# Performance work log

Measured on AMD Instinct MI355X. Metric: run time of the kernel, lower is better.

Reference implementation:

```python
import jax, jax.numpy as jnp
import numpy as np

B, D, H, W = 16, 512, 32, 32   # batch, input_dim, spatial
CD, K = 256, 8192              # codebook dim, num codes
COMMIT = 1.0


def setup_inputs() -> dict:
    key = jax.random.key(0)
    k0, k1, k2, k3 = jax.random.split(key, 4)
    x = jax.random.normal(k0, (B, D, H, W), dtype=jnp.float32)
    # project_in: Linear(D -> CD); project_out: Linear(CD -> D)
    W_in = jax.random.normal(k1, (CD, D), dtype=jnp.float32) * (1.0 / np.sqrt(D))
    b_in = jnp.zeros((CD,), dtype=jnp.float32)
    W_out = jax.random.normal(k2, (D, CD), dtype=jnp.float32) * (1.0 / np.sqrt(CD))
    b_out = jnp.zeros((D,), dtype=jnp.float32)
    codebook = jax.random.normal(k3, (K, CD), dtype=jnp.float32) * 0.05
    return {"x": x, "W_in": W_in, "b_in": b_in, "W_out": W_out,
            "b_out": b_out, "codebook": codebook}


def reference(x, W_in, b_in, W_out, b_out, codebook):
    b, d, h, w = x.shape
    # b d h w -> b (h w) d
    xt = x.reshape(b, d, h * w).transpose(0, 2, 1)
    z = xt @ W_in.T + b_in                              # [b, n, CD]
    # squared euclidean distances to all codes: ||z||^2 - 2 z.e + ||e||^2
    d2 = ((z * z).sum(-1, keepdims=True)
          - 2.0 * jnp.einsum('bnc,kc->bnk', z, codebook)
          + (codebook * codebook).sum(-1))              # [b, n, K]
    indices = jnp.argmin(d2, axis=-1)                   # [b, n] int
    q = codebook[indices]                               # [b, n, CD]
    # training branch: commitment loss + straight-through estimator
    commitment_loss = COMMIT * jnp.mean((jax.lax.stop_gradient(q) - z) ** 2)
    q_ste = z + jax.lax.stop_gradient(q - z)
    out = q_ste @ W_out.T + b_out                       # [b, n, d]
    out = out.transpose(0, 2, 1).reshape(b, d, h, w)    # b (h w) d -> b d h w
    return out, indices, commitment_loss
```

## Files before the change

kernel.cpp:

```cpp
#include <hip/hip_runtime.h>
#include <cfloat>
#include <cstdint>

#define B_      16
#define DIN     512
#define HW      1024
#define CDIM    256
#define KCODES  8192
#define NTOK    (B_ * HW)
#define OUT_ELEMS (B_ * DIN * HW)
#define GAP_EPS 1e-3f
#define NSTRIP  8
#define NPART   (NSTRIP * 2)
#define CPS     (KCODES / NSTRIP)
#define MAXR    4096
#define RCHUNK  32
#define RBLOCKS 2048
#define LOSS_SCALE (1.0f / ((float)NTOK * (float)CDIM))

typedef __attribute__((ext_vector_type(8))) short bf16x8;
typedef __attribute__((ext_vector_type(4))) float f32x4;

static __device__ __forceinline__ short f2bf(float f) {
  unsigned u = __builtin_bit_cast(unsigned, f);
  u += 0x7FFFu + ((u >> 16) & 1u);
  return (short)(u >> 16);
}
static __device__ __forceinline__ float bf2f(short h) {
  unsigned u = ((unsigned)(unsigned short)h) << 16;
  return __builtin_bit_cast(float, u);
}

#define GLL16(gsrc, ldst)                                                      \
  __builtin_amdgcn_global_load_lds(                                            \
      (const __attribute__((address_space(1))) unsigned int*)(gsrc),           \
      (__attribute__((address_space(3))) unsigned int*)(ldst), 16, 0, 0)

#define PREP_CB_BLKS 2048
#define PREP_W_BLKS  128
#define PREP_X_BLKS  2048
__global__ __launch_bounds__(256) void k_prep(
    const float* __restrict__ cb, const float* __restrict__ Win,
    const float* __restrict__ Wout, const float* __restrict__ x,
    short* __restrict__ cb_hi, short* __restrict__ cb_lo, float* __restrict__ ee,
    short* __restrict__ wi_hi, short* __restrict__ wi_lo,
    short* __restrict__ wo_hi, short* __restrict__ wo_lo,
    short* __restrict__ xT_hi, short* __restrict__ xT_lo,
    float* __restrict__ loss, int* __restrict__ rcount) {
  __shared__ float T[64][65];
  const int blk = blockIdx.x;
  const int tid = threadIdx.x;
  if (blk == 0 && tid < 2) {
    if (tid == 0) *loss = 0.0f; else *rcount = 0;
  }
  if (blk < PREP_CB_BLKS) {
    const int wid = (blk * 256 + tid) >> 6;
    const int lane = tid & 63;
    const float4 v = *(const float4*)(cb + (size_t)wid * CDIM + lane * 4);
    float s = v.x * v.x + v.y * v.y + v.z * v.z + v.w * v.w;
    short4 h, l;
    h.x = f2bf(v.x); l.x = f2bf(v.x - bf2f(h.x));
    h.y = f2bf(v.y); l.y = f2bf(v.y - bf2f(h.y));
    h.z = f2bf(v.z); l.z = f2bf(v.z - bf2f(h.z));
    h.w = f2bf(v.w); l.w = f2bf(v.w - bf2f(h.w));
    *(short4*)(cb_hi + (size_t)wid * CDIM + lane * 4) = h;
    *(short4*)(cb_lo + (size_t)wid * CDIM + lane * 4) = l;
#pragma unroll
    for (int off = 32; off > 0; off >>= 1) s += __shfl_down(s, off, 64);
    if (lane == 0) ee[wid] = s;
  } else if (blk < PREP_CB_BLKS + PREP_W_BLKS) {
    const int i = ((blk - PREP_CB_BLKS) * 256 + tid) * 4;
    {
      const float4 v = *(const float4*)(Win + i);
      short4 h, l;
      h.x = f2bf(v.x); l.x = f2bf(v.x - bf2f(h.x));
      h.y = f2bf(v.y); l.y = f2bf(v.y - bf2f(h.y));
      h.z = f2bf(v.z); l.z = f2bf(v.z - bf2f(h.z));
      h.w = f2bf(v.w); l.w = f2bf(v.w - bf2f(h.w));
      *(short4*)(wi_hi + i) = h; *(short4*)(wi_lo + i) = l;
    }
    {
      const float4 v = *(const float4*)(Wout + i);
      short4 h, l;
      h.x = f2bf(v.x); l.x = f2bf(v.x - bf2f(h.x));
      h.y = f2bf(v.y); l.y = f2bf(v.y - bf2f(h.y));
      h.z = f2bf(v.z); l.z = f2bf(v.z - bf2f(h.z));
      h.w = f2bf(v.w); l.w = f2bf(v.w - bf2f(h.w));
      *(short4*)(wo_hi + i) = h; *(short4*)(wo_lo + i) = l;
    }
  } else {
    const int id = blk - PREP_CB_BLKS - PREP_W_BLKS;
    const int xb = id & 255, yb = id >> 8;
    const int b = xb >> 4;
    const int hw0 = (xb & 15) * 64;
    const int din0 = yb * 64;
    {
      const int r = tid >> 2;
      const int c = tid & 3;
      const float* src = x + ((size_t)b * DIN + din0 + r) * HW + hw0 + c * 16;
#pragma unroll
      for (int j = 0; j < 4; ++j) {
        const float4 v = *(const float4*)(src + j * 4);
        T[r][c * 16 + j * 4 + 0] = v.x;
        T[r][c * 16 + j * 4 + 1] = v.y;
        T[r][c * 16 + j * 4 + 2] = v.z;
        T[r][c * 16 + j * 4 + 3] = v.w;
      }
    }
    __syncthreads();
    {
      const int tt = tid & 63;
      const int c2 = tid >> 6;
      short h[16], l[16];
#pragma unroll
      for (int j = 0; j < 16; ++j) {
        const float f = T[c2 * 16 + j][tt];
        h[j] = f2bf(f); l[j] = f2bf(f - bf2f(h[j]));
      }
      const size_t base = ((size_t)b * HW + hw0 + tt) * DIN + din0 + c2 * 16;
      *(bf16x8*)(xT_hi + base)     = *(bf16x8*)&h[0];
      *(bf16x8*)(xT_hi + base + 8) = *(bf16x8*)&h[8];
      *(bf16x8*)(xT_lo + base)     = *(bf16x8*)&l[0];
      *(bf16x8*)(xT_lo + base + 8) = *(bf16x8*)&l[8];
    }
  }
}

__global__ __launch_bounds__(256, 2) void k_proj_in_mfma(
    const short* __restrict__ xT_hi, const short* __restrict__ xT_lo,
    const short* __restrict__ wi_hi, const short* __restrict__ wi_lo,
    const float* __restrict__ bin,
    short* __restrict__ z_hi, short* __restrict__ z_lo) {
  __shared__ short lds_s[4 * 128 * 32];
  char* ldsc = (char*)lds_s;
  const int tid = threadIdx.x;
  const int w = tid >> 6, lane = tid & 63;
  const int quad = lane >> 4, l16 = lane & 15;
  const int wm = w >> 1, wn = w & 1;
  const int tok0 = blockIdx.x * 128;
  const int cd0 = blockIdx.y * 128;

  const int uA = (w << 6) + lane, uB = uA + 256;
  const int tA = uA >> 2, pA = uA & 3, qA = pA ^ ((tA >> 1) & 3);
  const int tB = uB >> 2, pB = uB & 3, qB = pB ^ ((tB >> 1) & 3);
  const int offA = tA * DIN + qA * 8;
  const int offB = tB * DIN + qB * 8;
  const short* gAh0 = xT_hi + (size_t)tok0 * DIN + offA;
  const short* gAh1 = xT_hi + (size_t)tok0 * DIN + offB;
  const short* gAl0 = xT_lo + (size_t)tok0 * DIN + offA;
  const short* gAl1 = xT_lo + (size_t)tok0 * DIN + offB;
  const short* gBh0 = wi_hi + (size_t)cd0 * DIN + offA;
  const short* gBh1 = wi_hi + (size_t)cd0 * DIN + offB;
  const short* gBl0 = wi_lo + (size_t)cd0 * DIN + offA;
  const short* gBl1 = wi_lo + (size_t)cd0 * DIN + offB;

  int aoffs[4], boffs[4];
#pragma unroll
  for (int mi = 0; mi < 4; ++mi) {
    const int t = wm * 64 + mi * 16 + l16;
    aoffs[mi] = t * 64 + (quad ^ ((t >> 1) & 3)) * 16;
  }
#pragma unroll
  for (int ni = 0; ni < 4; ++ni) {
    const int t = wn * 64 + ni * 16 + l16;
    boffs[ni] = 16384 + t * 64 + (quad ^ ((t >> 1) & 3)) * 16;
  }

  f32x4 acc[4][4];
#pragma unroll
  for (int mi = 0; mi < 4; ++mi)
#pragma unroll
    for (int ni = 0; ni < 4; ++ni) acc[mi][ni] = (f32x4){0.f, 0.f, 0.f, 0.f};

  for (int kb = 0; kb < DIN; kb += 32) {
    __syncthreads();
    GLL16(gAh0 + kb, ldsc + ((0 * 4 + w) << 10));
    GLL16(gAh1 + kb, ldsc + ((1 * 4 + w) << 10));
    GLL16(gAl0 + kb, ldsc + ((2 * 4 + w) << 10));
    GLL16(gAl1 + kb, ldsc + ((3 * 4 + w) << 10));
    GLL16(gBh0 + kb, ldsc + ((4 * 4 + w) << 10));
    GLL16(gBh1 + kb, ldsc + ((5 * 4 + w) << 10));
    GLL16(gBl0 + kb, ldsc + ((6 * 4 + w) << 10));
    GLL16(gBl1 + kb, ldsc + ((7 * 4 + w) << 10));
    __syncthreads();
    bf16x8 ah[4], al[4], bh[4], bl[4];
#pragma unroll
    for (int mi = 0; mi < 4; ++mi) {
      ah[mi] = *(const bf16x8*)(ldsc + aoffs[mi]);
      al[mi] = *(const bf16x8*)(ldsc + 8192 + aoffs[mi]);
    }
#pragma unroll
    for (int ni = 0; ni < 4; ++ni) {
      bh[ni] = *(const bf16x8*)(ldsc + boffs[ni]);
      bl[ni] = *(const bf16x8*)(ldsc + 8192 + boffs[ni]);
    }
#pragma unroll
    for (int mi = 0; mi < 4; ++mi)
#pragma unroll
      for (int ni = 0; ni < 4; ++ni) {
        f32x4 c = acc[mi][ni];
        c = __builtin_amdgcn_mfma_f32_16x16x32_bf16(ah[mi], bh[ni], c, 0, 0, 0);
        c = __builtin_amdgcn_mfma_f32_16x16x32_bf16(ah[mi], bl[ni], c, 0, 0, 0);
        c = __builtin_amdgcn_mfma_f32_16x16x32_bf16(al[mi], bh[ni], c, 0, 0, 0);
        acc[mi][ni] = c;
      }
  }
  float bv[4];
#pragma unroll
  for (int ni = 0; ni < 4; ++ni) bv[ni] = bin[cd0 + wn * 64 + ni * 16 + l16];
#pragma unroll
  for (int mi = 0; mi < 4; ++mi)
#pragma unroll
    for (int r = 0; r < 4; ++r) {
      const int t = tok0 + wm * 64 + mi * 16 + quad * 4 + r;
#pragma unroll
      for (int ni = 0; ni < 4; ++ni) {
        const int cd = cd0 + wn * 64 + ni * 16 + l16;
        const float o = acc[mi][ni][r] + bv[ni];
        const short h = f2bf(o);
        z_hi[(size_t)t * CDIM + cd] = h;
        z_lo[(size_t)t * CDIM + cd] = f2bf(o - bf2f(h));
      }
    }
}

__global__ __launch_bounds__(256, 2) void k_argmin_mfma(
    const short* __restrict__ z_hi, const short* __restrict__ z_lo,
    const short* __restrict__ cb_hi, const short* __restrict__ cb_lo,
    const float* __restrict__ ee,
    float* __restrict__ pmv, int* __restrict__ pmi, float* __restrict__ psv) {
  __shared__ short lds_s[4 * 128 * 32];
  char* ldsc = (char*)lds_s;
  const int tid = threadIdx.x;
  const int w = tid >> 6, lane = tid & 63;
  const int quad = lane >> 4, l16 = lane & 15;
  const int wm = w >> 1, wn = w & 1;
  const int tok0 = blockIdx.x * 128;
  const int cbase = blockIdx.y * CPS;

  const int uA = (w << 6) + lane, uB = uA + 256;
  const int tA = uA >> 2, pA = uA & 3, qA = pA ^ ((tA >> 1) & 3);
  const int tB = uB >> 2, pB = uB & 3, qB = pB ^ ((tB >> 1) & 3);
  const int offA = tA * CDIM + qA * 8;
  const int offB = tB * CDIM + qB * 8;
  const short* gAh0 = z_hi + (size_t)tok0 * CDIM + offA;
  const short* gAh1 = z_hi + (size_t)tok0 * CDIM + offB;
  const short* gAl0 = z_lo + (size_t)tok0 * CDIM + offA;
  const short* gAl1 = z_lo + (size_t)tok0 * CDIM + offB;

  int aoffs[4], boffs[4];
#pragma unroll
  for (int mi = 0; mi < 4; ++mi) {
    const int t = wm * 64 + mi * 16 + l16;
    aoffs[mi] = t * 64 + (quad ^ ((t >> 1) & 3)) * 16;
  }
#pragma unroll
  for (int ni = 0; ni < 4; ++ni) {
    const int t = wn * 64 + ni * 16 + l16;
    boffs[ni] = 16384 + t * 64 + (quad ^ ((t >> 1) & 3)) * 16;
  }

  float mv[16], sv[16]; int bidx[16];
#pragma unroll
  for (int j = 0; j < 16; ++j) { mv[j] = FLT_MAX; sv[j] = FLT_MAX; bidx[j] = 0; }

  for (int ct = 0; ct < CPS / 128; ++ct) {
    const int ctile = cbase + ct * 128;
    const short* gBh0 = cb_hi + (size_t)ctile * CDIM + offA;
    const short* gBh1 = cb_hi + (size_t)ctile * CDIM + offB;
    const short* gBl0 = cb_lo + (size_t)ctile * CDIM + offA;
    const short* gBl1 = cb_lo + (size_t)ctile * CDIM + offB;
    f32x4 acc[4][4];
#pragma unroll
    for (int mi = 0; mi < 4; ++mi)
#pragma unroll
      for (int ni = 0; ni < 4; ++ni) acc[mi][ni] = (f32x4){0.f, 0.f, 0.f, 0.f};

    for (int kb = 0; kb < CDIM; kb += 32) {
      __syncthreads();
      GLL16(gAh0 + kb, ldsc + ((0 * 4 + w) << 10));
      GLL16(gAh1 + kb, ldsc + ((1 * 4 + w) << 10));
      GLL16(gAl0 + kb, ldsc + ((2 * 4 + w) << 10));
      GLL16(gAl1 + kb, ldsc + ((3 * 4 + w) << 10));
      GLL16(gBh0 + kb, ldsc + ((4 * 4 + w) << 10));
      GLL16(gBh1 + kb, ldsc + ((5 * 4 + w) << 10));
      GLL16(gBl0 + kb, ldsc + ((6 * 4 + w) << 10));
      GLL16(gBl1 + kb, ldsc + ((7 * 4 + w) << 10));
      __syncthreads();
      bf16x8 ah[4], al[4], bh[4], bl[4];
#pragma unroll
      for (int mi = 0; mi < 4; ++mi) {
        ah[mi] = *(const bf16x8*)(ldsc + aoffs[mi]);
        al[mi] = *(const bf16x8*)(ldsc + 8192 + aoffs[mi]);
      }
#pragma unroll
      for (int ni = 0; ni < 4; ++ni) {
        bh[ni] = *(const bf16x8*)(ldsc + boffs[ni]);
        bl[ni] = *(const bf16x8*)(ldsc + 8192 + boffs[ni]);
      }
#pragma unroll
      for (int mi = 0; mi < 4; ++mi)
#pragma unroll
        for (int ni = 0; ni < 4; ++ni) {
          f32x4 c = acc[mi][ni];
          c = __builtin_amdgcn_mfma_f32_16x16x32_bf16(ah[mi], bh[ni], c, 0, 0, 0);
          c = __builtin_amdgcn_mfma_f32_16x16x32_bf16(ah[mi], bl[ni], c, 0, 0, 0);
          c = __builtin_amdgcn_mfma_f32_16x16x32_bf16(al[mi], bh[ni], c, 0, 0, 0);
          acc[mi][ni] = c;
        }
    }
    float eev[4];
#pragma unroll
    for (int ni = 0; ni < 4; ++ni) eev[ni] = ee[ctile + wn * 64 + ni * 16 + l16];
    const int cb2 = ctile + wn * 64 + l16;
#pragma unroll
    for (int mi = 0; mi < 4; ++mi)
#pragma unroll
      for (int r = 0; r < 4; ++r) {
        const int j = mi * 4 + r;
#pragma unroll
        for (int ni = 0; ni < 4; ++ni) {
          const float s = fmaf(-2.0f, acc[mi][ni][r], eev[ni]);
          sv[j] = fminf(sv[j], fmaxf(mv[j], s));
          if (s < mv[j]) { mv[j] = s; bidx[j] = cb2 + ni * 16; }
        }
      }
  }
#pragma unroll
  for (int off = 1; off < 16; off <<= 1) {
#pragma unroll
    for (int j = 0; j < 16; ++j) {
      const float ov = __shfl_xor(mv[j], off, 64);
      const int   oi = __shfl_xor(bidx[j], off, 64);
      const float os = __shfl_xor(sv[j], off, 64);
      const float snew = fminf(fminf(sv[j], os), fmaxf(mv[j], ov));
      if (ov < mv[j] || (ov == mv[j] && oi < bidx[j])) { mv[j] = ov; bidx[j] = oi; }
      sv[j] = snew;
    }
  }
  if (l16 == 0) {
    const int strip = blockIdx.y * 2 + wn;
#pragma unroll
    for (int j = 0; j < 16; ++j) {
      const int mi = j >> 2, r = j & 3;
      const int t = tok0 + wm * 64 + mi * 16 + quad * 4 + r;
      const size_t o = (size_t)strip * NTOK + t;
      pmv[o] = mv[j]; pmi[o] = bidx[j]; psv[o] = sv[j];
    }
  }
}

__global__ __launch_bounds__(256) void k_merge_loss(
    const float* __restrict__ pmv, const int* __restrict__ pmi,
    const float* __restrict__ psv,
    const short* __restrict__ z_hi, const short* __restrict__ z_lo,
    const float* __restrict__ cb,
    int* __restrict__ idxi, float* __restrict__ idx_f,
    int* __restrict__ rlist, int* __restrict__ rcount,
    float* __restrict__ loss) {
  __shared__ float lpart[4];
  const int tid = threadIdx.x;
  const int wv = tid >> 6, lane = tid & 63;
  const int t = blockIdx.x * 4 + wv;
  float mv = FLT_MAX, sv = FLT_MAX; int mi = 0x7fffffff;
  if (lane < NPART) {
    mv = pmv[(size_t)lane * NTOK + t];
    mi = pmi[(size_t)lane * NTOK + t];
    sv = psv[(size_t)lane * NTOK + t];
  }
#pragma unroll
  for (int off = 1; off < 16; off <<= 1) {
    const float ov = __shfl_xor(mv, off, 64);
    const int   oi = __shfl_xor(mi, off, 64);
    const float os = __shfl_xor(sv, off, 64);
    const float snew = fminf(fminf(sv, os), fmaxf(mv, ov));
    if (ov < mv || (ov == mv && oi < mi)) { mv = ov; mi = oi; }
    sv = snew;
  }
  const int mif = __shfl(mi, 0, 64);
  const short4 h4 = *(const short4*)(z_hi + (size_t)t * CDIM + lane * 4);
  const short4 l4 = *(const short4*)(z_lo + (size_t)t * CDIM + lane * 4);
  const float4 qv = *(const float4*)(cb + (size_t)mif * CDIM + lane * 4);
  const float dx = qv.x - (bf2f(h4.x) + bf2f(l4.x));
  const float dy = qv.y - (bf2f(h4.y) + bf2f(l4.y));
  const float dz = qv.z - (bf2f(h4.z) + bf2f(l4.z));
  const float dw = qv.w - (bf2f(h4.w) + bf2f(l4.w));
  float s = dx * dx + dy * dy + dz * dz + dw * dw;
#pragma unroll
  for (int off = 32; off > 0; off >>= 1) s += __shfl_down(s, off, 64);
  if (lane == 0) {
    idxi[t] = mif;
    idx_f[t] = (float)mif;
    lpart[wv] = s;
    if (sv - mv < GAP_EPS) {
      const int pos = atomicAdd(rcount, 1);
      if (pos < MAXR) rlist[pos] = t;
    }
  }
  __syncthreads();
  if (tid == 0) {
    atomicAdd(loss, (lpart[0] + lpart[1] + lpart[2] + lpart[3]) * LOSS_SCALE);
  }
}

__global__ __launch_bounds__(256) void k_rescue_chunk(
    const short* __restrict__ z_hi, const short* __restrict__ z_lo,
    const float* __restrict__ cb,
    const int* __restrict__ rlist, const int* __restrict__ rcount,
    double* __restrict__ slotv, int* __restrict__ sloti) {
  const int cnt0 = *rcount;
  const int cnt = cnt0 < MAXR ? cnt0 : MAXR;
  const int li0 = blockIdx.x >> 5;
  const int chunk = blockIdx.x & (RCHUNK - 1);
  if (li0 >= cnt) return;
  __shared__ float zrow[CDIM];
  __shared__ double rv[256];
  __shared__ int ri[256];
  const int tid = threadIdx.x;
  for (int li = li0; li < cnt; li += RBLOCKS / RCHUNK) {
    const int t = rlist[li];
    zrow[tid] = bf2f(z_hi[(size_t)t * CDIM + tid]) + bf2f(z_lo[(size_t)t * CDIM + tid]);
    __syncthreads();
    const int k = chunk * 256 + tid;
    const float* e = cb + (size_t)k * CDIM;
    double s0 = 0.0, s1 = 0.0, s2 = 0.0, s3 = 0.0;
    for (int c = 0; c < CDIM; c += 4) {
      const double d0 = (double)zrow[c]     - (double)e[c];
      const double d1 = (double)zrow[c + 1] - (double)e[c + 1];
      const double d2 = (double)zrow[c + 2] - (double)e[c + 2];
      const double d3 = (double)zrow[c + 3] - (double)e[c + 3];
      s0 += d0 * d0; s1 += d1 * d1; s2 += d2 * d2; s3 += d3 * d3;
    }
    rv[tid] = (s0 + s1) + (s2 + s3);
    ri[tid] = k;
    __syncthreads();
    for (int off = 128; off > 0; off >>= 1) {
      if (tid < off) {
        if (rv[tid + off] < rv[tid] ||
            (rv[tid + off] == rv[tid] && ri[tid + off] < ri[tid])) {
          rv[tid] = rv[tid + off]; ri[tid] = ri[tid + off];
        }
      }
      __syncthreads();
    }
    if (tid == 0) {
      slotv[(size_t)li * RCHUNK + chunk] = rv[0];
      sloti[(size_t)li * RCHUNK + chunk] = ri[0];
    }
    __syncthreads();
  }
}

__global__ __launch_bounds__(256) void k_rescue_fin(
    const double* __restrict__ slotv, const int* __restrict__ sloti,
    const int* __restrict__ rlist, const int* __restrict__ rcount,
    const short* __restrict__ z_hi, const short* __restrict__ z_lo,
    const float* __restrict__ cb,
    int* __restrict__ idxi, float* __restrict__ idx_f, float* __restrict__ loss) {
  const int cnt0 = *rcount;
  const int cnt = cnt0 < MAXR ? cnt0 : MAXR;
  const int tid = threadIdx.x;
  const int wv = tid >> 6, lane = tid & 63;
  for (int li = wv; li < cnt; li += 4) {
    double bv = 1e300; int bx = 0x7fffffff;
    if (lane < RCHUNK) {
      bv = slotv[(size_t)li * RCHUNK + lane];
      bx = sloti[(size_t)li * RCHUNK + lane];
    }
#pragma unroll
    for (int off = 1; off < 32; off <<= 1) {
      const double ov = __shfl_xor(bv, off, 64);
      const int   oi = __shfl_xor(bx, off, 64);
      if (ov < bv || (ov == bv && oi < bx)) { bv = ov; bx = oi; }
    }
    const int newi = __shfl(bx, 0, 64);
    const int t = rlist[li];
    const int oldi = idxi[t];
    if (newi != oldi) {
      const short4 h4 = *(const short4*)(z_hi + (size_t)t * CDIM + lane * 4);
      const short4 l4 = *(const short4*)(z_lo + (size_t)t * CDIM + lane * 4);
      const float4 qn = *(const float4*)(cb + (size_t)newi * CDIM + lane * 4);
      const float4 qo = *(const float4*)(cb + (size_t)oldi * CDIM + lane * 4);
      const float zx = bf2f(h4.x) + bf2f(l4.x);
      const float zy = bf2f(h4.y) + bf2f(l4.y);
      const float zz = bf2f(h4.z) + bf2f(l4.z);
      const float zw = bf2f(h4.w) + bf2f(l4.w);
      float d = (qn.x - zx) * (qn.x - zx) - (qo.x - zx) * (qo.x - zx)
              + (qn.y - zy) * (qn.y - zy) - (qo.y - zy) * (qo.y - zy)
              + (qn.z - zz) * (qn.z - zz) - (qo.z - zz) * (qo.z - zz)
              + (qn.w - zw) * (qn.w - zw) - (qo.w - zw) * (qo.w - zw);
#pragma unroll
      for (int off = 32; off > 0; off >>= 1) d += __shfl_down(d, off, 64);
      if (lane == 0) {
        idxi[t] = newi;
        idx_f[t] = (float)newi;
        atomicAdd(loss, d * LOSS_SCALE);
      }
    }
  }
}

__global__ __launch_bounds__(256, 2) void k_proj_out_mfma(
    const short* __restrict__ wo_hi, const short* __restrict__ wo_lo,
    const short* __restrict__ cb_hi, const short* __restrict__ cb_lo,
    const int* __restrict__ idxi, const float* __restrict__ bout,
    float* __restrict__ out) {
  __shared__ short lds_s[4 * 128 * 32];
  char* ldsc = (char*)lds_s;
  const int tid = threadIdx.x;
  const int w = tid >> 6, lane = tid & 63;
  const int quad = lane >> 4, l16 = lane & 15;
  const int wm = w >> 1, wn = w & 1;
  const int tok0 = blockIdx.x * 128;
  const int din0 = blockIdx.y * 128;

  const int uA = (w << 6) + lane, uB = uA + 256;
  const int tA = uA >> 2, pA = uA & 3, qA = pA ^ ((tA >> 1) & 3);
  const int tB = uB >> 2, pB = uB & 3, qB = pB ^ ((tB >> 1) & 3);
  const short* gAh0 = wo_hi + (size_t)(din0 + tA) * CDIM + qA * 8;
  const short* gAh1 = wo_hi + (size_t)(din0 + tB) * CDIM + qB * 8;
  const short* gAl0 = wo_lo + (size_t)(din0 + tA) * CDIM + qA * 8;
  const short* gAl1 = wo_lo + (size_t)(din0 + tB) * CDIM + qB * 8;
  const int iA = idxi[tok0 + tA];
  const int iB = idxi[tok0 + tB];
  const short* gBh0 = cb_hi + (size_t)iA * CDIM + qA * 8;
  const short* gBh1 = cb_hi + (size_t)iB * CDIM + qB * 8;
  const short* gBl0 = cb_lo + (size_t)iA * CDIM + qA * 8;
  const short* gBl1 = cb_lo + (size_t)iB * CDIM + qB * 8;

  int aoffs[4], boffs[4];
#pragma unroll
  for (int mi = 0; mi < 4; ++mi) {
    const int t = wm * 64 + mi * 16 + l16;
    aoffs[mi] = t * 64 + (quad ^ ((t >> 1) & 3)) * 16;
  }
#pragma unroll
  for (int ni = 0; ni < 4; ++ni) {
    const int t = wn * 64 + ni * 16 + l16;
    boffs[ni] = 16384 + t * 64 + (quad ^ ((t >> 1) & 3)) * 16;
  }

  f32x4 acc[4][4];
#pragma unroll
  for (int mi = 0; mi < 4; ++mi)
#pragma unroll
    for (int ni = 0; ni < 4; ++ni) acc[mi][ni] = (f32x4){0.f, 0.f, 0.f, 0.f};

  for (int kb = 0; kb < CDIM; kb += 32) {
    __syncthreads();
    GLL16(gAh0 + kb, ldsc + ((0 * 4 + w) << 10));
    GLL16(gAh1 + kb, ldsc + ((1 * 4 + w) << 10));
    GLL16(gAl0 + kb, ldsc + ((2 * 4 + w) << 10));
    GLL16(gAl1 + kb, ldsc + ((3 * 4 + w) << 10));
    GLL16(gBh0 + kb, ldsc + ((4 * 4 + w) << 10));
    GLL16(gBh1 + kb, ldsc + ((5 * 4 + w) << 10));
    GLL16(gBl0 + kb, ldsc + ((6 * 4 + w) << 10));
    GLL16(gBl1 + kb, ldsc + ((7 * 4 + w) << 10));
    __syncthreads();
    bf16x8 ah[4], al[4], bh[4], bl[4];
#pragma unroll
    for (int mi = 0; mi < 4; ++mi) {
      ah[mi] = *(const bf16x8*)(ldsc + aoffs[mi]);
      al[mi] = *(const bf16x8*)(ldsc + 8192 + aoffs[mi]);
    }
#pragma unroll
    for (int ni = 0; ni < 4; ++ni) {
      bh[ni] = *(const bf16x8*)(ldsc + boffs[ni]);
      bl[ni] = *(const bf16x8*)(ldsc + 8192 + boffs[ni]);
    }
#pragma unroll
    for (int mi = 0; mi < 4; ++mi)
#pragma unroll
      for (int ni = 0; ni < 4; ++ni) {
        f32x4 c = acc[mi][ni];
        c = __builtin_amdgcn_mfma_f32_16x16x32_bf16(ah[mi], bh[ni], c, 0, 0, 0);
        c = __builtin_amdgcn_mfma_f32_16x16x32_bf16(ah[mi], bl[ni], c, 0, 0, 0);
        c = __builtin_amdgcn_mfma_f32_16x16x32_bf16(al[mi], bh[ni], c, 0, 0, 0);
        acc[mi][ni] = c;
      }
  }
  const int b = tok0 >> 10;
  const int hwb = tok0 & (HW - 1);
  float* ob = out + (size_t)b * DIN * HW;
#pragma unroll
  for (int mi = 0; mi < 4; ++mi)
#pragma unroll
    for (int r = 0; r < 4; ++r) {
      const int din = din0 + wm * 64 + mi * 16 + quad * 4 + r;
      const float bb = bout[din];
#pragma unroll
      for (int ni = 0; ni < 4; ++ni) {
        const int hw = hwb + wn * 64 + ni * 16 + l16;
        ob[(size_t)din * HW + hw] = acc[mi][ni][r] + bb;
      }
    }
}

extern "C" void kernel_launch(void* const* d_in, const int* in_sizes, int n_in,
                              void* d_out, int out_size, void* d_ws, size_t ws_size,
                              hipStream_t stream) {
  const float* x    = (const float*)d_in[0];
  const float* Win  = (const float*)d_in[1];
  const float* bin  = (const float*)d_in[2];
  const float* Wout = (const float*)d_in[3];
  const float* bout = (const float*)d_in[4];
  const float* cb   = (const float*)d_in[5];

  float* out   = (float*)d_out;
  float* idx_f = out + OUT_ELEMS;
  float* loss  = out + OUT_ELEMS + NTOK;

  char* w = (char*)d_ws;
  size_t off = 0;
  short* z_hi  = (short*)(w + off); off += (size_t)NTOK * CDIM * 2;
  short* z_lo  = (short*)(w + off); off += (size_t)NTOK * CDIM * 2;
  short* cb_hi = (short*)(w + off); off += (size_t)KCODES * CDIM * 2;
  short* cb_lo = (short*)(w + off); off += (size_t)KCODES * CDIM * 2;
  short* xT_hi = (short*)(w + off); off += (size_t)NTOK * DIN * 2;
  short* xT_lo = (short*)(w + off); off += (size_t)NTOK * DIN * 2;
  short* wi_hi = (short*)(w + off); off += (size_t)CDIM * DIN * 2;
  short* wi_lo = (short*)(w + off); off += (size_t)CDIM * DIN * 2;
  short* wo_hi = (short*)(w + off); off += (size_t)DIN * CDIM * 2;
  short* wo_lo = (short*)(w + off); off += (size_t)DIN * CDIM * 2;
  float* ee    = (float*)(w + off); off += (size_t)KCODES * 4;
  int*   idxi  = (int*)(w + off);   off += (size_t)NTOK * 4;
  float* pmv   = (float*)(w + off); off += (size_t)NPART * NTOK * 4;
  int*   pmi   = (int*)(w + off);   off += (size_t)NPART * NTOK * 4;
  float* psv   = (float*)(w + off); off += (size_t)NPART * NTOK * 4;
  int*   rlist = (int*)(w + off);   off += (size_t)MAXR * 4;
  int*   rcount= (int*)(w + off);   off += 256;
  double* slotv= (double*)(w + off);off += (size_t)MAXR * RCHUNK * 8;
  int*   sloti = (int*)(w + off);   off += (size_t)MAXR * RCHUNK * 4;

  k_prep        <<<dim3(PREP_CB_BLKS + PREP_W_BLKS + PREP_X_BLKS),
                   dim3(256), 0, stream>>>(cb, Win, Wout, x, cb_hi, cb_lo, ee,
                                           wi_hi, wi_lo, wo_hi, wo_lo,
                                           xT_hi, xT_lo, loss, rcount);
  k_proj_in_mfma<<<dim3(NTOK / 128, CDIM / 128), dim3(256), 0, stream>>>(
      xT_hi, xT_lo, wi_hi, wi_lo, bin, z_hi, z_lo);
  k_argmin_mfma <<<dim3(NTOK / 128, NSTRIP), dim3(256), 0, stream>>>(
      z_hi, z_lo, cb_hi, cb_lo, ee, pmv, pmi, psv);
  k_merge_loss  <<<dim3(NTOK / 4), dim3(256), 0, stream>>>(
      pmv, pmi, psv, z_hi, z_lo, cb, idxi, idx_f, rlist, rcount, loss);
  k_rescue_chunk<<<dim3(RBLOCKS), dim3(256), 0, stream>>>(
      z_hi, z_lo, cb, rlist, rcount, slotv, sloti);
  k_rescue_fin  <<<dim3(1), dim3(256), 0, stream>>>(
      slotv, sloti, rlist, rcount, z_hi, z_lo, cb, idxi, idx_f, loss);
  k_proj_out_mfma<<<dim3(NTOK / 128, DIN / 128), dim3(256), 0, stream>>>(
      wo_hi, wo_lo, cb_hi, cb_lo, idxi, bout, out);
}
```

Measured before the change: 467.0 us.

## Switch split-precision GEMMs from bf16 to scaled fp16 and drop low-part terms

```diff
diff --git a/kernel.cpp b/kernel.cpp
--- a/kernel.cpp
+++ b/kernel.cpp
@@ -9,31 +9,33 @@
 #define KCODES  8192
 #define NTOK    (B_ * HW)
 #define OUT_ELEMS (B_ * DIN * HW)
-#define GAP_EPS 1e-3f
+#define GAP_EPS 5e-3f
 #define NSTRIP  8
 #define NPART   (NSTRIP * 2)
 #define CPS     (KCODES / NSTRIP)
 #define MAXR    4096
 #define RCHUNK  32
-#define RBLOCKS 2048
+#define RBLOCKS 8192
 #define LOSS_SCALE (1.0f / ((float)NTOK * (float)CDIM))
-
-typedef __attribute__((ext_vector_type(8))) short bf16x8;
+#define WSCALE      16.0f
+#define INV_WS      0.0625f
+#define INV_WS2     0.00390625f
+#define NEG2_INV_WS (-0.125f)
+
+typedef __attribute__((ext_vector_type(8))) _Float16 f16x8;
 typedef __attribute__((ext_vector_type(4))) float f32x4;
 
-static __device__ __forceinline__ short f2bf(float f) {
-  unsigned u = __builtin_bit_cast(unsigned, f);
-  u += 0x7FFFu + ((u >> 16) & 1u);
-  return (short)(u >> 16);
-}
-static __device__ __forceinline__ float bf2f(short h) {
-  unsigned u = ((unsigned)(unsigned short)h) << 16;
-  return __builtin_bit_cast(float, u);
+static __device__ __forceinline__ short f2h(float f) {
+  _Float16 h = (_Float16)f;
+  return __builtin_bit_cast(short, h);
+}
+static __device__ __forceinline__ float h2f(short h) {
+  return (float)__builtin_bit_cast(_Float16, h);
 }
 
 #define GLL16(gsrc, ldst)                                                      \
-  __builtin_amdgcn_global_load_lds(                                            \
-      (const __attribute__((address_space(1))) unsigned int*)(gsrc),           \
+  __builtin_amdgcn_global_load_lds(                                           \
+      (const __attribute__((address_space(1))) unsigned int*)(gsrc),          \
       (__attribute__((address_space(3))) unsigned int*)(ldst), 16, 0, 0)
 
 #define PREP_CB_BLKS 2048
@@ -58,11 +60,13 @@
     const int lane = tid & 63;
     const float4 v = *(const float4*)(cb + (size_t)wid * CDIM + lane * 4);
     float s = v.x * v.x + v.y * v.y + v.z * v.z + v.w * v.w;
+    const float sx = v.x * WSCALE, sy = v.y * WSCALE,
+                sz = v.z * WSCALE, sw = v.w * WSCALE;
     short4 h, l;
-    h.x = f2bf(v.x); l.x = f2bf(v.x - bf2f(h.x));
-    h.y = f2bf(v.y); l.y = f2bf(v.y - bf2f(h.y));
-    h.z = f2bf(v.z); l.z = f2bf(v.z - bf2f(h.z));
-    h.w = f2bf(v.w); l.w = f2bf(v.w - bf2f(h.w));
+    h.x = f2h(sx); l.x = f2h(sx - h2f(h.x));
+    h.y = f2h(sy); l.y = f2h(sy - h2f(h.y));
+    h.z = f2h(sz); l.z = f2h(sz - h2f(h.z));
+    h.w = f2h(sw); l.w = f2h(sw - h2f(h.w));
     *(short4*)(cb_hi + (size_t)wid * CDIM + lane * 4) = h;
     *(short4*)(cb_lo + (size_t)wid * CDIM + lane * 4) = l;
 #pragma unroll
@@ -72,20 +76,24 @@
     const int i = ((blk - PREP_CB_BLKS) * 256 + tid) * 4;
     {
       const float4 v = *(const float4*)(Win + i);
+      const float sx = v.x * WSCALE, sy = v.y * WSCALE,
+                  sz = v.z * WSCALE, sw = v.w * WSCALE;
       short4 h, l;
-      h.x = f2bf(v.x); l.x = f2bf(v.x - bf2f(h.x));
-      h.y = f2bf(v.y); l.y = f2bf(v.y - bf2f(h.y));
-      h.z = f2bf(v.z); l.z = f2bf(v.z - bf2f(h.z));
-      h.w = f2bf(v.w); l.w = f2bf(v.w - bf2f(h.w));
+      h.x = f2h(sx); l.x = f2h(sx - h2f(h.x));
+      h.y = f2h(sy); l.y = f2h(sy - h2f(h.y));
+      h.z = f2h(sz); l.z = f2h(sz - h2f(h.z));
+      h.w = f2h(sw); l.w = f2h(sw - h2f(h.w));
       *(short4*)(wi_hi + i) = h; *(short4*)(wi_lo + i) = l;
     }
     {
       const float4 v = *(const float4*)(Wout + i);
+      const float sx = v.x * WSCALE, sy = v.y * WSCALE,
+                  sz = v.z * WSCALE, sw = v.w * WSCALE;
       short4 h, l;
-      h.x = f2bf(v.x); l.x = f2bf(v.x - bf2f(h.x));
-      h.y = f2bf(v.y); l.y = f2bf(v.y - bf2f(h.y));
-      h.z = f2bf(v.z); l.z = f2bf(v.z - bf2f(h.z));
-      h.w = f2bf(v.w); l.w = f2bf(v.w - bf2f(h.w));
+      h.x = f2h(sx); l.x = f2h(sx - h2f(h.x));
+      h.y = f2h(sy); l.y = f2h(sy - h2f(h.y));
+      h.z = f2h(sz); l.z = f2h(sz - h2f(h.z));
+      h.w = f2h(sw); l.w = f2h(sw - h2f(h.w));
       *(short4*)(wo_hi + i) = h; *(short4*)(wo_lo + i) = l;
     }
   } else {
@@ -115,13 +123,13 @@
 #pragma unroll
       for (int j = 0; j < 16; ++j) {
         const float f = T[c2 * 16 + j][tt];
-        h[j] = f2bf(f); l[j] = f2bf(f - bf2f(h[j]));
+        h[j] = f2h(f); l[j] = f2h(f - h2f(h[j]));
       }
       const size_t base = ((size_t)b * HW + hw0 + tt) * DIN + din0 + c2 * 16;
-      *(bf16x8*)(xT_hi + base)     = *(bf16x8*)&h[0];
-      *(bf16x8*)(xT_hi + base + 8) = *(bf16x8*)&h[8];
-      *(bf16x8*)(xT_lo + base)     = *(bf16x8*)&l[0];
-      *(bf16x8*)(xT_lo + base + 8) = *(bf16x8*)&l[8];
+      *(f16x8*)(xT_hi + base)     = *(f16x8*)&h[0];
+      *(f16x8*)(xT_hi + base + 8) = *(f16x8*)&h[8];
+      *(f16x8*)(xT_lo + base)     = *(f16x8*)&l[0];
+      *(f16x8*)(xT_lo + base + 8) = *(f16x8*)&l[8];
     }
   }
 }
@@ -183,25 +191,25 @@
     GLL16(gBl0 + kb, ldsc + ((6 * 4 + w) << 10));
     GLL16(gBl1 + kb, ldsc + ((7 * 4 + w) << 10));
     __syncthreads();
-    bf16x8 ah[4], al[4], bh[4], bl[4];
+    f16x8 ah[4], al[4], bh[4], bl[4];
 #pragma unroll
     for (int mi = 0; mi < 4; ++mi) {
-      ah[mi] = *(const bf16x8*)(ldsc + aoffs[mi]);
-      al[mi] = *(const bf16x8*)(ldsc + 8192 + aoffs[mi]);
+      ah[mi] = *(const f16x8*)(ldsc + aoffs[mi]);
+      al[mi] = *(const f16x8*)(ldsc + 8192 + aoffs[mi]);
     }
 #pragma unroll
     for (int ni = 0; ni < 4; ++ni) {
-      bh[ni] = *(const bf16x8*)(ldsc + boffs[ni]);
-      bl[ni] = *(const bf16x8*)(ldsc + 8192 + boffs[ni]);
+      bh[ni] = *(const f16x8*)(ldsc + boffs[ni]);
+      bl[ni] = *(const f16x8*)(ldsc + 8192 + boffs[ni]);
     }
 #pragma unroll
     for (int mi = 0; mi < 4; ++mi)
 #pragma unroll
       for (int ni = 0; ni < 4; ++ni) {
         f32x4 c = acc[mi][ni];
-        c = __builtin_amdgcn_mfma_f32_16x16x32_bf16(ah[mi], bh[ni], c, 0, 0, 0);
-        c = __builtin_amdgcn_mfma_f32_16x16x32_bf16(ah[mi], bl[ni], c, 0, 0, 0);
-        c = __builtin_amdgcn_mfma_f32_16x16x32_bf16(al[mi], bh[ni], c, 0, 0, 0);
+        c = __builtin_amdgcn_mfma_f32_16x16x32_f16(ah[mi], bh[ni], c, 0, 0, 0);
+        c = __builtin_amdgcn_mfma_f32_16x16x32_f16(ah[mi], bl[ni], c, 0, 0, 0);
+        c = __builtin_amdgcn_mfma_f32_16x16x32_f16(al[mi], bh[ni], c, 0, 0, 0);
         acc[mi][ni] = c;
       }
   }
@@ -216,20 +224,20 @@
 #pragma unroll
       for (int ni = 0; ni < 4; ++ni) {
         const int cd = cd0 + wn * 64 + ni * 16 + l16;
-        const float o = acc[mi][ni][r] + bv[ni];
-        const short h = f2bf(o);
+        const float o = acc[mi][ni][r] * INV_WS + bv[ni];
+        const short h = f2h(o);
         z_hi[(size_t)t * CDIM + cd] = h;
-        z_lo[(size_t)t * CDIM + cd] = f2bf(o - bf2f(h));
+        z_lo[(size_t)t * CDIM + cd] = f2h(o - h2f(h));
       }
     }
 }
 
 __global__ __launch_bounds__(256, 2) void k_argmin_mfma(
-    const short* __restrict__ z_hi, const short* __restrict__ z_lo,
+    const short* __restrict__ z_hi,
     const short* __restrict__ cb_hi, const short* __restrict__ cb_lo,
     const float* __restrict__ ee,
     float* __restrict__ pmv, int* __restrict__ pmi, float* __restrict__ psv) {
-  __shared__ short lds_s[4 * 128 * 32];
+  __shared__ short lds_s[3 * 128 * 32];
   char* ldsc = (char*)lds_s;
   const int tid = threadIdx.x;
   const int w = tid >> 6, lane = tid & 63;
@@ -245,8 +253,6 @@
   const int offB = tB * CDIM + qB * 8;
   const short* gAh0 = z_hi + (size_t)tok0 * CDIM + offA;
   const short* gAh1 = z_hi + (size_t)tok0 * CDIM + offB;
-  const short* gAl0 = z_lo + (size_t)tok0 * CDIM + offA;
-  const short* gAl1 = z_lo + (size_t)tok0 * CDIM + offB;
 
   int aoffs[4], boffs[4];
 #pragma unroll
@@ -257,7 +263,7 @@
 #pragma unroll
   for (int ni = 0; ni < 4; ++ni) {
     const int t = wn * 64 + ni * 16 + l16;
-    boffs[ni] = 16384 + t * 64 + (quad ^ ((t >> 1) & 3)) * 16;
+    boffs[ni] = 8192 + t * 64 + (quad ^ ((t >> 1) & 3)) * 16;
   }
 
   float mv[16], sv[16]; int bidx[16];
@@ -280,32 +286,27 @@
       __syncthreads();
       GLL16(gAh0 + kb, ldsc + ((0 * 4 + w) << 10));
       GLL16(gAh1 + kb, ldsc + ((1 * 4 + w) << 10));
-      GLL16(gAl0 + kb, ldsc + ((2 * 4 + w) << 10));
-      GLL16(gAl1 + kb, ldsc + ((3 * 4 + w) << 10));
-      GLL16(gBh0 + kb, ldsc + ((4 * 4 + w) << 10));
-      GLL16(gBh1 + kb, ldsc + ((5 * 4 + w) << 10));
-      GLL16(gBl0 + kb, ldsc + ((6 * 4 + w) << 10));
-      GLL16(gBl1 + kb, ldsc + ((7 * 4 + w) << 10));
+      GLL16(gBh0 + kb, ldsc + ((2 * 4 + w) << 10));
+      GLL16(gBh1 + kb, ldsc + ((3 * 4 + w) << 10));
+      GLL16(gBl0 + kb, ldsc + ((4 * 4 + w) << 10));
+      GLL16(gBl1 + kb, ldsc + ((5 * 4 + w) << 10));
       __syncthreads();
-      bf16x8 ah[4], al[4], bh[4], bl[4];
-#pragma unroll
-      for (int mi = 0; mi < 4; ++mi) {
-        ah[mi] = *(const bf16x8*)(ldsc + aoffs[mi]);
-        al[mi] = *(const bf16x8*)(ldsc + 8192 + aoffs[mi]);
-      }
+      f16x8 ah[4], bh[4], bl[4];
+#pragma unroll
+      for (int mi = 0; mi < 4; ++mi)
+        ah[mi] = *(const f16x8*)(ldsc + aoffs[mi]);
 #pragma unroll
       for (int ni = 0; ni < 4; ++ni) {
-        bh[ni] = *(const bf16x8*)(ldsc + boffs[ni]);
-        bl[ni] = *(const bf16x8*)(ldsc + 8192 + boffs[ni]);
+        bh[ni] = *(const f16x8*)(ldsc + boffs[ni]);
+        bl[ni] = *(const f16x8*)(ldsc + 8192 + boffs[ni]);
       }
 #pragma unroll
       for (int mi = 0; mi < 4; ++mi)
 #pragma unroll
         for (int ni = 0; ni < 4; ++ni) {
           f32x4 c = acc[mi][ni];
-          c = __builtin_amdgcn_mfma_f32_16x16x32_bf16(ah[mi], bh[ni], c, 0, 0, 0);
-          c = __builtin_amdgcn_mfma_f32_16x16x32_bf16(ah[mi], bl[ni], c, 0, 0, 0);
-          c = __builtin_amdgcn_mfma_f32_16x16x32_bf16(al[mi], bh[ni], c, 0, 0, 0);
+          c = __builtin_amdgcn_mfma_f32_16x16x32_f16(ah[mi], bh[ni], c, 0, 0, 0);
+          c = __builtin_amdgcn_mfma_f32_16x16x32_f16(ah[mi], bl[ni], c, 0, 0, 0);
           acc[mi][ni] = c;
         }
     }
@@ -320,7 +321,7 @@
         const int j = mi * 4 + r;
 #pragma unroll
         for (int ni = 0; ni < 4; ++ni) {
-          const float s = fmaf(-2.0f, acc[mi][ni][r], eev[ni]);
+          const float s = fmaf(NEG2_INV_WS, acc[mi][ni][r], eev[ni]);
           sv[j] = fminf(sv[j], fmaxf(mv[j], s));
           if (s < mv[j]) { mv[j] = s; bidx[j] = cb2 + ni * 16; }
         }
@@ -381,10 +382,10 @@
   const short4 h4 = *(const short4*)(z_hi + (size_t)t * CDIM + lane * 4);
   const short4 l4 = *(const short4*)(z_lo + (size_t)t * CDIM + lane * 4);
   const float4 qv = *(const float4*)(cb + (size_t)mif * CDIM + lane * 4);
-  const float dx = qv.x - (bf2f(h4.x) + bf2f(l4.x));
-  const float dy = qv.y - (bf2f(h4.y) + bf2f(l4.y));
-  const float dz = qv.z - (bf2f(h4.z) + bf2f(l4.z));
-  const float dw = qv.w - (bf2f(h4.w) + bf2f(l4.w));
+  const float dx = qv.x - (h2f(h4.x) + h2f(l4.x));
+  const float dy = qv.y - (h2f(h4.y) + h2f(l4.y));
+  const float dz = qv.z - (h2f(h4.z) + h2f(l4.z));
+  const float dw = qv.w - (h2f(h4.w) + h2f(l4.w));
   float s = dx * dx + dy * dy + dz * dz + dw * dw;
 #pragma unroll
   for (int off = 32; off > 0; off >>= 1) s += __shfl_down(s, off, 64);
@@ -419,16 +420,17 @@
   const int tid = threadIdx.x;
   for (int li = li0; li < cnt; li += RBLOCKS / RCHUNK) {
     const int t = rlist[li];
-    zrow[tid] = bf2f(z_hi[(size_t)t * CDIM + tid]) + bf2f(z_lo[(size_t)t * CDIM + tid]);
+    zrow[tid] = h2f(z_hi[(size_t)t * CDIM + tid]) + h2f(z_lo[(size_t)t * CDIM + tid]);
     __syncthreads();
     const int k = chunk * 256 + tid;
     const float* e = cb + (size_t)k * CDIM;
     double s0 = 0.0, s1 = 0.0, s2 = 0.0, s3 = 0.0;
     for (int c = 0; c < CDIM; c += 4) {
-      const double d0 = (double)zrow[c]     - (double)e[c];
-      const double d1 = (double)zrow[c + 1] - (double)e[c + 1];
-      const double d2 = (double)zrow[c + 2] - (double)e[c + 2];
-      const double d3 = (double)zrow[c + 3] - (double)e[c + 3];
+      const float4 ev = *(const float4*)(e + c);
+      const double d0 = (double)zrow[c]     - (double)ev.x;
+      const double d1 = (double)zrow[c + 1] - (double)ev.y;
+      const double d2 = (double)zrow[c + 2] - (double)ev.z;
+      const double d3 = (double)zrow[c + 3] - (double)ev.w;
       s0 += d0 * d0; s1 += d1 * d1; s2 += d2 * d2; s3 += d3 * d3;
     }
     rv[tid] = (s0 + s1) + (s2 + s3);
@@ -481,10 +483,10 @@
       const short4 l4 = *(const short4*)(z_lo + (size_t)t * CDIM + lane * 4);
       const float4 qn = *(const float4*)(cb + (size_t)newi * CDIM + lane * 4);
       const float4 qo = *(const float4*)(cb + (size_t)oldi * CDIM + lane * 4);
-      const float zx = bf2f(h4.x) + bf2f(l4.x);
-      const float zy = bf2f(h4.y) + bf2f(l4.y);
-      const float zz = bf2f(h4.z) + bf2f(l4.z);
-      const float zw = bf2f(h4.w) + bf2f(l4.w);
+      const float zx = h2f(h4.x) + h2f(l4.x);
+      const float zy = h2f(h4.y) + h2f(l4.y);
+      const float zz = h2f(h4.z) + h2f(l4.z);
+      const float zw = h2f(h4.w) + h2f(l4.w);
       float d = (qn.x - zx) * (qn.x - zx) - (qo.x - zx) * (qo.x - zx)
               + (qn.y - zy) * (qn.y - zy) - (qo.y - zy) * (qo.y - zy)
               + (qn.z - zz) * (qn.z - zz) - (qo.z - zz) * (qo.z - zz)
@@ -501,11 +503,11 @@
 }
 
 __global__ __launch_bounds__(256, 2) void k_proj_out_mfma(
-    const short* __restrict__ wo_hi, const short* __restrict__ wo_lo,
+    const short* __restrict__ wo_hi,
     const short* __restrict__ cb_hi, const short* __restrict__ cb_lo,
     const int* __restrict__ idxi, const float* __restrict__ bout,
     float* __restrict__ out) {
-  __shared__ short lds_s[4 * 128 * 32];
+  __shared__ short lds_s[3 * 128 * 32];
   char* ldsc = (char*)lds_s;
   const int tid = threadIdx.x;
   const int w = tid >> 6, lane = tid & 63;
@@ -519,8 +521,6 @@
   const int tB = uB >> 2, pB = uB & 3, qB = pB ^ ((tB >> 1) & 3);
   const short* gAh0 = wo_hi + (size_t)(din0 + tA) * CDIM + qA * 8;
   const short* gAh1 = wo_hi + (size_t)(din0 + tB) * CDIM + qB * 8;
-  const short* gAl0 = wo_lo + (size_t)(din0 + tA) * CDIM + qA * 8;
-  const short* gAl1 = wo_lo + (size_t)(din0 + tB) * CDIM + qB * 8;
   const int iA = idxi[tok0 + tA];
   const int iB = idxi[tok0 + tB];
   const short* gBh0 = cb_hi + (size_t)iA * CDIM + qA * 8;
@@ -537,7 +537,7 @@
 #pragma unroll
   for (int ni = 0; ni < 4; ++ni) {
     const int t = wn * 64 + ni * 16 + l16;
-    boffs[ni] = 16384 + t * 64 + (quad ^ ((t >> 1) & 3)) * 16;
+    boffs[ni] = 8192 + t * 64 + (quad ^ ((t >> 1) & 3)) * 16;
   }
 
   f32x4 acc[4][4];
@@ -550,32 +550,27 @@
     __syncthreads();
     GLL16(gAh0 + kb, ldsc + ((0 * 4 + w) << 10));
     GLL16(gAh1 + kb, ldsc + ((1 * 4 + w) << 10));
-    GLL16(gAl0 + kb, ldsc + ((2 * 4 + w) << 10));
-    GLL16(gAl1 + kb, ldsc + ((3 * 4 + w) << 10));
-    GLL16(gBh0 + kb, ldsc + ((4 * 4 + w) << 10));
-    GLL16(gBh1 + kb, ldsc + ((5 * 4 + w) << 10));
-    GLL16(gBl0 + kb, ldsc + ((6 * 4 + w) << 10));
-    GLL16(gBl1 + kb, ldsc + ((7 * 4 + w) << 10));
-    __syncthreads();
-    bf16x8 ah[4], al[4], bh[4], bl[4];
-#pragma unroll
-    for (int mi = 0; mi < 4; ++mi) {
-      ah[mi] = *(const bf16x8*)(ldsc + aoffs[mi]);
-      al[mi] = *(const bf16x8*)(ldsc + 8192 + aoffs[mi]);
-    }
+    GLL16(gBh0 + kb, ldsc + ((2 * 4 + w) << 10));
+    GLL16(gBh1 + kb, ldsc + ((3 * 4 + w) << 10));
+    GLL16(gBl0 + kb, ldsc + ((4 * 4 + w) << 10));
+    GLL16(gBl1 + kb, ldsc + ((5 * 4 + w) << 10));
+    __syncthreads();
+    f16x8 ah[4], bh[4], bl[4];
+#pragma unroll
+    for (int mi = 0; mi < 4; ++mi)
+      ah[mi] = *(const f16x8*)(ldsc + aoffs[mi]);
 #pragma unroll
     for (int ni = 0; ni < 4; ++ni) {
-      bh[ni] = *(const bf16x8*)(ldsc + boffs[ni]);
-      bl[ni] = *(const bf16x8*)(ldsc + 8192 + boffs[ni]);
+      bh[ni] = *(const f16x8*)(ldsc + boffs[ni]);
+      bl[ni] = *(const f16x8*)(ldsc + 8192 + boffs[ni]);
     }
 #pragma unroll
     for (int mi = 0; mi < 4; ++mi)
 #pragma unroll
       for (int ni = 0; ni < 4; ++ni) {
         f32x4 c = acc[mi][ni];
-        c = __builtin_amdgcn_mfma_f32_16x16x32_bf16(ah[mi], bh[ni], c, 0, 0, 0);
-        c = __builtin_amdgcn_mfma_f32_16x16x32_bf16(ah[mi], bl[ni], c, 0, 0, 0);
-        c = __builtin_amdgcn_mfma_f32_16x16x32_bf16(al[mi], bh[ni], c, 0, 0, 0);
+        c = __builtin_amdgcn_mfma_f32_16x16x32_f16(ah[mi], bh[ni], c, 0, 0, 0);
+        c = __builtin_amdgcn_mfma_f32_16x16x32_f16(ah[mi], bl[ni], c, 0, 0, 0);
         acc[mi][ni] = c;
       }
   }
@@ -591,7 +586,7 @@
 #pragma unroll
       for (int ni = 0; ni < 4; ++ni) {
         const int hw = hwb + wn * 64 + ni * 16 + l16;
-        ob[(size_t)din * HW + hw] = acc[mi][ni][r] + bb;
+        ob[(size_t)din * HW + hw] = acc[mi][ni][r] * INV_WS2 + bb;
       }
     }
 }
@@ -639,7 +634,7 @@
   k_proj_in_mfma<<<dim3(NTOK / 128, CDIM / 128), dim3(256), 0, stream>>>(
       xT_hi, xT_lo, wi_hi, wi_lo, bin, z_hi, z_lo);
   k_argmin_mfma <<<dim3(NTOK / 128, NSTRIP), dim3(256), 0, stream>>>(
-      z_hi, z_lo, cb_hi, cb_lo, ee, pmv, pmi, psv);
+      z_hi, cb_hi, cb_lo, ee, pmv, pmi, psv);
   k_merge_loss  <<<dim3(NTOK / 4), dim3(256), 0, stream>>>(
       pmv, pmi, psv, z_hi, z_lo, cb, idxi, idx_f, rlist, rcount, loss);
   k_rescue_chunk<<<dim3(RBLOCKS), dim3(256), 0, stream>>>(
@@ -647,5 +642,5 @@
   k_rescue_fin  <<<dim3(1), dim3(256), 0, stream>>>(
       slotv, sloti, rlist, rcount, z_hi, z_lo, cb, idxi, idx_f, loss);
   k_proj_out_mfma<<<dim3(NTOK / 128, DIN / 128), dim3(256), 0, stream>>>(
-      wo_hi, wo_lo, cb_hi, cb_lo, idxi, bout, out);
-}
+      wo_hi, cb_hi, cb_lo, idxi, bout, out);
+}
```

New measurement: 591.2 us. +26.6%, slower.
